# Performance work log

Measured on AMD Instinct MI355X. Metric: run time of the kernel, lower is better.

The kernel has to match this reference:

```python
import jax, jax.numpy as jnp
import numpy as np

B, S, D, H = 2, 2048, 1024, 16
HD = D // H  # head_dim = 64
SCALE = HD ** -0.5


def setup_inputs() -> dict:
    key = jax.random.key(0)
    ks = jax.random.split(key, 10)
    std = D ** -0.5
    return {
        "x": jax.random.normal(ks[0], (B, S, D), jnp.float32),
        "y": jax.random.normal(ks[1], (B, S, D), jnp.float32),
        "Wq": jax.random.normal(ks[2], (D, D), jnp.float32) * std,
        "bq": jnp.zeros((D,), jnp.float32),
        "Wk": jax.random.normal(ks[3], (D, D), jnp.float32) * std,
        "bk": jnp.zeros((D,), jnp.float32),
        "Wv": jax.random.normal(ks[4], (D, D), jnp.float32) * std,
        "bv": jnp.zeros((D,), jnp.float32),
        "Wo": jax.random.normal(ks[5], (D, D), jnp.float32) * std,
        "bo": jnp.zeros((D,), jnp.float32),
    }


def reference(x, y, Wq, bq, Wk, bk, Wv, bv, Wo, bo):
    # Linear projections (torch Linear: x @ W.T + b; here W stored as [in,out])
    q = x @ Wq + bq  # [B,S,D]
    k = y @ Wk + bk
    v = y @ Wv + bv
    # split heads -> [B,H,S,hd]
    q = q.reshape(B, S, H, HD).transpose(0, 2, 1, 3)
    k = k.reshape(B, S, H, HD).transpose(0, 2, 1, 3)
    v = v.reshape(B, S, H, HD).transpose(0, 2, 1, 3)
    scores = jnp.einsum("bhqd,bhkd->bhqk", q, k) * SCALE  # [B,H,S,S]
    causal = jnp.tril(jnp.ones((S, S), dtype=bool))  # keep lower triangle
    scores = jnp.where(causal[None, None], scores, -jnp.inf)
    attn = jax.nn.softmax(scores, axis=-1)
    out = jnp.einsum("bhqk,bhkd->bhqd", attn, v)  # [B,H,S,hd]
    out = out.transpose(0, 2, 1, 3).reshape(B, S, D)
    return out @ Wo + bo
```

## Files before the change

kernel.cpp:

```cpp
#include <hip/hip_runtime.h>
#include <hip/hip_bf16.h>


#define BDIM 2
#define SDIM 2048
#define DDIM 1024
#define HDIM 16
#define HD   64
#define MDIM (BDIM*SDIM)
#define C2 0.18033688011112042f

using short8  = __attribute__((ext_vector_type(8))) short;
using floatx4 = __attribute__((ext_vector_type(4))) float;

static __device__ __forceinline__ unsigned short f2bf(float x) {
    union { float f; unsigned int u; } c; c.f = x;
    unsigned int r = (c.u + 0x7fffu + ((c.u >> 16) & 1u)) >> 16;
    return (unsigned short)r;
}

static __device__ __forceinline__ unsigned int pack2bf(float a, float b) {
    union { float f; unsigned int u; } ua, ub;
    ua.f = a; ub.f = b;
    return __builtin_amdgcn_perm(ub.u + 0x8000u, ua.u + 0x8000u, 0x07060302u);
}

#define GLD16(g, l) __builtin_amdgcn_global_load_lds(                        \
    (const __attribute__((address_space(1))) void*)(g),                      \
    (__attribute__((address_space(3))) void*)(l), 16, 0, 0)

__global__ __launch_bounds__(256) void prep_kernel(
    const float* __restrict__ X, const float* __restrict__ Y,
    const float* __restrict__ W0, const float* __restrict__ W1,
    const float* __restrict__ W2, const float* __restrict__ W3,
    unsigned short* __restrict__ Xo, unsigned short* __restrict__ Yo,
    unsigned short* __restrict__ T0, unsigned short* __restrict__ T1,
    unsigned short* __restrict__ T2, unsigned short* __restrict__ T3)
{
    __shared__ float tile[64][68];
    const int z = blockIdx.z;
    const int t = threadIdx.x;
    if (z < 2) {
        const float* A    = z ? Y : X;
        unsigned short* O = z ? Yo : Xo;
        const int idx = blockIdx.x * 256 + t;
        const float4 a = ((const float4*)A)[idx*2];
        const float4 b = ((const float4*)A)[idx*2 + 1];
        ushort4 lo, hi;
        lo.x = f2bf(a.x); lo.y = f2bf(a.y); lo.z = f2bf(a.z); lo.w = f2bf(a.w);
        hi.x = f2bf(b.x); hi.y = f2bf(b.y); hi.z = f2bf(b.z); hi.w = f2bf(b.w);
        ((ushort4*)O)[idx*2]     = lo;
        ((ushort4*)O)[idx*2 + 1] = hi;
        return;
    }
    if (blockIdx.x >= 256) return;
    const int zz = z - 2;
    const float* W    = (zz == 0) ? W0 : (zz == 1) ? W1 : (zz == 2) ? W2 : W3;
    unsigned short* T = (zz == 0) ? T0 : (zz == 1) ? T1 : (zz == 2) ? T2 : T3;
    const int k0 = (blockIdx.x & 15) * 64, n0 = (blockIdx.x >> 4) * 64;
    #pragma unroll
    for (int i = 0; i < 4; ++i) {
        const int idx = t + i*256;
        const int kr = idx >> 4, c4 = idx & 15;
        float4 v = *(const float4*)&W[(size_t)(k0 + kr) * DDIM + n0 + c4*4];
        tile[kr][c4*4+0] = v.x; tile[kr][c4*4+1] = v.y;
        tile[kr][c4*4+2] = v.z; tile[kr][c4*4+3] = v.w;
    }
    __syncthreads();
    #pragma unroll
    for (int i = 0; i < 4; ++i) {
        const int idx = t + i*256;
        const int nr = idx >> 4, kc = idx & 15;
        ushort4 o;
        o.x = f2bf(tile[kc*4+0][nr]); o.y = f2bf(tile[kc*4+1][nr]);
        o.z = f2bf(tile[kc*4+2][nr]); o.w = f2bf(tile[kc*4+3][nr]);
        *(ushort4*)&T[(size_t)(n0 + nr) * DDIM + k0 + kc*4] = o;
    }
}

template <bool SWAP>
__device__ __forceinline__ void gemm128_core(
    const unsigned short* __restrict__ A, const unsigned short* __restrict__ Bt,
    int bm, int bn, unsigned short* As, unsigned short* Bs, floatx4 acc[4][4])
{
    const int t = threadIdx.x;
    const int w = t >> 6, l = t & 63;
    const int quad = l >> 4, col = l & 15;
    const int wr = (w >> 1) * 64, wc = (w & 1) * 64;

    const int c1 = t + 256;
    const int r0 = t >> 2,  o0 = (t & 3) * 8;
    const int r1 = c1 >> 2, o1 = (c1 & 3) * 8;

    const unsigned short* Ar0 = A  + (size_t)(bm + r0) * DDIM + o0;
    const unsigned short* Ar1 = A  + (size_t)(bm + r1) * DDIM + o1;
    const unsigned short* Br0 = Bt + (size_t)(bn + r0) * DDIM + o0;
    const unsigned short* Br1 = Bt + (size_t)(bn + r1) * DDIM + o1;

    GLD16(Ar0, As + t*8);
    GLD16(Ar1, As + c1*8);
    GLD16(Br0, Bs + t*8);
    GLD16(Br1, Bs + c1*8);

    for (int kt = 0; kt < DDIM; kt += 32) {
        const int cur = (kt >> 5) & 1;
        unsigned short* Asn = As + (cur ^ 1) * 4096;
        unsigned short* Bsn = Bs + (cur ^ 1) * 4096;
        __syncthreads();
        if (kt + 32 < DDIM) {
            GLD16(Ar0 + kt + 32, Asn + t*8);
            GLD16(Ar1 + kt + 32, Asn + c1*8);
            GLD16(Br0 + kt + 32, Bsn + t*8);
            GLD16(Br1 + kt + 32, Bsn + c1*8);
        }
        const unsigned short* Asc = As + cur*4096;
        const unsigned short* Bsc = Bs + cur*4096;
        short8 af[4], bfr[4];
        #pragma unroll
        for (int i = 0; i < 4; ++i)
            af[i] = *(const short8*)&Asc[(wr + i*16 + col)*32 + quad*8];
        #pragma unroll
        for (int j = 0; j < 4; ++j)
            bfr[j] = *(const short8*)&Bsc[(wc + j*16 + col)*32 + quad*8];
        #pragma unroll
        for (int i = 0; i < 4; ++i)
            #pragma unroll
            for (int j = 0; j < 4; ++j)
                acc[i][j] = SWAP
                    ? __builtin_amdgcn_mfma_f32_16x16x32_bf16(bfr[j], af[i], acc[i][j], 0, 0, 0)
                    : __builtin_amdgcn_mfma_f32_16x16x32_bf16(af[i], bfr[j], acc[i][j], 0, 0, 0);
    }
}

__global__ __launch_bounds__(256) void qkv_gemm_kernel(
    const unsigned short* __restrict__ xbf, const unsigned short* __restrict__ ybf,
    const unsigned short* __restrict__ Wqt, const unsigned short* __restrict__ Wkt,
    const unsigned short* __restrict__ Wvt,
    const float* __restrict__ bq, const float* __restrict__ bk,
    const float* __restrict__ bv,
    unsigned short* __restrict__ Qbf, unsigned short* __restrict__ Kbf,
    unsigned short* __restrict__ vT)
{
    __shared__ __align__(16) unsigned short As[2*4096];
    __shared__ __align__(16) unsigned short Bs[2*4096];

    const int z = blockIdx.z;
    const unsigned short* A  = (z == 0) ? xbf : ybf;
    const unsigned short* Wt = (z == 0) ? Wqt : (z == 1) ? Wkt : Wvt;
    const float* bp          = (z == 0) ? bq  : (z == 1) ? bk  : bv;

    const int bm = (blockIdx.x * 4 + (blockIdx.y & 3)) * 128;
    const int bn = (blockIdx.y >> 2) * 128;

    const int t = threadIdx.x;
    const int w = t >> 6, l = t & 63;
    const int quad = l >> 4, col = l & 15;
    const int wr = (w >> 1) * 64, wc = (w & 1) * 64;

    floatx4 acc[4][4] = {};

    if (z < 2) {
        gemm128_core<true>(A, Wt, bm, bn, As, Bs, acc);
        unsigned short* O = (z == 0) ? Qbf : Kbf;
        const float sc = (z == 0) ? C2 : 1.0f;
        float4 bias4[4];
        #pragma unroll
        for (int j = 0; j < 4; ++j)
            bias4[j] = *(const float4*)&bp[bn + wc + j*16 + quad*4];
        #pragma unroll
        for (int i = 0; i < 4; ++i) {
            const int m = bm + wr + i*16 + col;
            unsigned short* rowp = O + (size_t)m * DDIM;
            #pragma unroll
            for (int j = 0; j < 4; ++j) {
                const float v0 = (acc[i][j][0] + bias4[j].x) * sc;
                const float v1 = (acc[i][j][1] + bias4[j].y) * sc;
                const float v2 = (acc[i][j][2] + bias4[j].z) * sc;
                const float v3 = (acc[i][j][3] + bias4[j].w) * sc;
                uint2 pk;
                pk.x = pack2bf(v0, v1);
                pk.y = pack2bf(v2, v3);
                *(uint2*)&rowp[bn + wc + j*16 + quad*4] = pk;
            }
        }
    } else {
        gemm128_core<false>(A, Wt, bm, bn, As, Bs, acc);
        #pragma unroll
        for (int j = 0; j < 4; ++j) {
            const int gn = bn + wc + j*16 + col;
            const float bias = bp[gn];
            #pragma unroll
            for (int i = 0; i < 4; ++i) {
                const int gm0 = bm + wr + i*16 + quad*4;
                uint2 pk;
                pk.x = pack2bf(acc[i][j][0] + bias, acc[i][j][1] + bias);
                pk.y = pack2bf(acc[i][j][2] + bias, acc[i][j][3] + bias);
                *(uint2*)&vT[((size_t)((gm0 >> 11) * DDIM + gn)) * SDIM + (gm0 & 2047)] = pk;
            }
        }
    }
}

__global__ __launch_bounds__(256) void out_gemm_kernel(
    const unsigned short* __restrict__ Obf, const unsigned short* __restrict__ Wot,
    const float* __restrict__ bo, float* __restrict__ out)
{
    __shared__ __align__(16) unsigned short As[2*4096];
    __shared__ __align__(16) unsigned short Bs[2*2048];

    const int t = threadIdx.x;
    const int w = t >> 6, l = t & 63;
    const int quad = l >> 4, col = l & 15;

    const int j  = (blockIdx.x >> 3) + 2 * blockIdx.y;
    const int bm = ((blockIdx.x & 7) * 4 + (j & 3)) * 128;
    const int bn = (j >> 2) * 64;

    const int wr = (w >> 1) * 64, wc = (w & 1) * 32;

    const int r0 = t >> 2, o0 = (t & 3) * 8;
    const unsigned short* Ar0 = Obf + (size_t)(bm + r0) * DDIM + o0;
    const unsigned short* Ar1 = Obf + (size_t)(bm + 64 + r0) * DDIM + o0;
    const unsigned short* Br  = Wot + (size_t)(bn + r0) * DDIM + o0;

    floatx4 acc[4][2] = {};

    GLD16(Ar0, As + t*8);
    GLD16(Ar1, As + (t + 256)*8);
    GLD16(Br,  Bs + t*8);

    for (int kt = 0; kt < DDIM; kt += 32) {
        const int cur = (kt >> 5) & 1;
        unsigned short* Asn = As + (cur ^ 1) * 4096;
        unsigned short* Bsn = Bs + (cur ^ 1) * 2048;
        __syncthreads();
        if (kt + 32 < DDIM) {
            GLD16(Ar0 + kt + 32, Asn + t*8);
            GLD16(Ar1 + kt + 32, Asn + (t + 256)*8);
            GLD16(Br  + kt + 32, Bsn + t*8);
        }
        const unsigned short* Asc = As + cur*4096;
        const unsigned short* Bsc = Bs + cur*2048;
        short8 af[4], bfr[2];
        #pragma unroll
        for (int i = 0; i < 4; ++i)
            af[i] = *(const short8*)&Asc[(wr + i*16 + col)*32 + quad*8];
        #pragma unroll
        for (int j2 = 0; j2 < 2; ++j2)
            bfr[j2] = *(const short8*)&Bsc[(wc + j2*16 + col)*32 + quad*8];
        #pragma unroll
        for (int i = 0; i < 4; ++i)
            #pragma unroll
            for (int j2 = 0; j2 < 2; ++j2)
                acc[i][j2] = __builtin_amdgcn_mfma_f32_16x16x32_bf16(
                    bfr[j2], af[i], acc[i][j2], 0, 0, 0);
    }

    float4 bias4[2];
    #pragma unroll
    for (int j2 = 0; j2 < 2; ++j2)
        bias4[j2] = *(const float4*)&bo[bn + wc + j2*16 + quad*4];
    #pragma unroll
    for (int i = 0; i < 4; ++i) {
        const int m = bm + wr + i*16 + col;
        float* rowp = out + (size_t)m * DDIM;
        #pragma unroll
        for (int j2 = 0; j2 < 2; ++j2) {
            float4 o;
            o.x = acc[i][j2][0] + bias4[j2].x;
            o.y = acc[i][j2][1] + bias4[j2].y;
            o.z = acc[i][j2][2] + bias4[j2].z;
            o.w = acc[i][j2][3] + bias4[j2].w;
            *(float4*)&rowp[bn + wc + j2*16 + quad*4] = o;
        }
    }
}

__global__ __launch_bounds__(256, 2) void attn_mfma_kernel(
    const unsigned short* __restrict__ Qbf, const unsigned short* __restrict__ Kbf,
    const unsigned short* __restrict__ vT, unsigned short* __restrict__ Obf)
{
    __shared__ float ls[2][4*64];
    __shared__ __align__(16) floatx4 os[2][1024];

    const int t = threadIdx.x;
    const int w = t >> 6, l = t & 63;
    const int quad = l >> 4, col = l & 15;

    const int lin = blockIdx.x;
    const int j   = lin >> 3, rem = j & 3;
    const int qt  = 31 - (j >> 2);
    const int b   = rem & 1;
    const int h   = (lin & 7) + 8 * (rem >> 1);

    const size_t hoff = (size_t)h * HD;
    const size_t bS   = (size_t)b * SDIM;
    const size_t bD   = (size_t)b * DDIM;
    const int qb = qt * 64;

    short8 qf[4][2];
    #pragma unroll
    for (int m = 0; m < 4; ++m)
        #pragma unroll
        for (int hf = 0; hf < 2; ++hf)
            qf[m][hf] = *(const short8*)
                &Qbf[(bS + qb + m*16 + col) * DDIM + hoff + hf*32 + quad*8];

    floatx4 o[4][4] = {};
    float lrun[4] = {0.f, 0.f, 0.f, 0.f};

    const int rowp = ((col >> 2) << 3) | (col & 3);
    const unsigned short* kb0 = Kbf + bS * DDIM + hoff + quad*8;
    const unsigned short* vb0 = vT + (bD + hoff + col) * SDIM + quad*8;

    #pragma unroll 1
    for (int it = w; it <= qt; it += 4) {
        const int ktb = it * 64;
        const bool diag = (it == qt);

        short8 kf[2][2][2];
        #pragma unroll
        for (int c = 0; c < 2; ++c)
            #pragma unroll
            for (int tt = 0; tt < 2; ++tt) {
                const size_t row = (size_t)(ktb + c*32 + tt*4 + rowp);
                kf[c][tt][0] = *(const short8*)&kb0[row * DDIM];
                kf[c][tt][1] = *(const short8*)&kb0[row * DDIM + 32];
            }
        short8 vf[4][2];
        #pragma unroll
        for (int n = 0; n < 4; ++n)
            #pragma unroll
            for (int c = 0; c < 2; ++c)
                vf[n][c] = *(const short8*)
                    &vb0[(size_t)(n*16) * SDIM + ktb + c*32];

        #pragma unroll
        for (int m = 0; m < 4; ++m) {
            #pragma unroll
            for (int c = 0; c < 2; ++c) {
                if (diag && (c*32 > m*16 + 15)) continue;
                const bool needm = diag && (c*32 + 31 > m*16);

                floatx4 s0 = {}, s1 = {};
                __builtin_amdgcn_s_setprio(1);
                s0 = __builtin_amdgcn_mfma_f32_16x16x32_bf16(kf[c][0][0], qf[m][0], s0, 0, 0, 0);
                s0 = __builtin_amdgcn_mfma_f32_16x16x32_bf16(kf[c][0][1], qf[m][1], s0, 0, 0, 0);
                s1 = __builtin_amdgcn_mfma_f32_16x16x32_bf16(kf[c][1][0], qf[m][0], s1, 0, 0, 0);
                s1 = __builtin_amdgcn_mfma_f32_16x16x32_bf16(kf[c][1][1], qf[m][1], s1, 0, 0, 0);
                __builtin_amdgcn_s_setprio(0);

                float p0[4], p1[4];
                const int qrow = m*16 + col;
                const int kls  = c*32 + quad*8;
                #pragma unroll
                for (int r = 0; r < 4; ++r) {
                    p0[r] = (needm && (kls + r     > qrow)) ? 0.0f : exp2f(s0[r]);
                    p1[r] = (needm && (kls + 4 + r > qrow)) ? 0.0f : exp2f(s1[r]);
                }
                lrun[m] += ((p0[0]+p0[1]) + (p0[2]+p0[3]))
                         + ((p1[0]+p1[1]) + (p1[2]+p1[3]));

                union { short8 v; unsigned int u[4]; } pf;
                pf.u[0] = pack2bf(p0[0], p0[1]);
                pf.u[1] = pack2bf(p0[2], p0[3]);
                pf.u[2] = pack2bf(p1[0], p1[1]);
                pf.u[3] = pack2bf(p1[2], p1[3]);

                __builtin_amdgcn_s_setprio(1);
                #pragma unroll
                for (int n = 0; n < 4; ++n)
                    o[n][m] = __builtin_amdgcn_mfma_f32_16x16x32_bf16(
                        vf[n][c], pf.v, o[n][m], 0, 0, 0);
                __builtin_amdgcn_s_setprio(0);
            }
        }
    }

    if (w >= 2) {
        const int s = w - 2;
        #pragma unroll
        for (int n = 0; n < 4; ++n)
            #pragma unroll
            for (int m = 0; m < 4; ++m)
                os[s][(n*4 + m)*64 + l] = o[n][m];
        #pragma unroll
        for (int m = 0; m < 4; ++m)
            ls[s][m*64 + l] = lrun[m];
    }
    __syncthreads();
    if (w < 2) {
        #pragma unroll
        for (int n = 0; n < 4; ++n)
            #pragma unroll
            for (int m = 0; m < 4; ++m)
                o[n][m] += os[w][(n*4 + m)*64 + l];
        #pragma unroll
        for (int m = 0; m < 4; ++m)
            lrun[m] += ls[w][m*64 + l];
    }
    __syncthreads();
    if (w == 1) {
        #pragma unroll
        for (int n = 0; n < 4; ++n)
            #pragma unroll
            for (int m = 0; m < 4; ++m)
                os[0][(n*4 + m)*64 + l] = o[n][m];
        #pragma unroll
        for (int m = 0; m < 4; ++m)
            ls[0][m*64 + l] = lrun[m];
    }
    __syncthreads();
    if (w == 0) {
        #pragma unroll
        for (int m = 0; m < 4; ++m) {
            float lt = lrun[m] + ls[0][m*64 + l];
            lt += __shfl_xor(lt, 16);
            lt += __shfl_xor(lt, 32);
            const float inv = 1.0f / lt;
            #pragma unroll
            for (int n = 0; n < 4; ++n) {
                const floatx4 ov = o[n][m] + os[0][(n*4 + m)*64 + l];
                uint2 pk;
                pk.x = pack2bf(ov[0] * inv, ov[1] * inv);
                pk.y = pack2bf(ov[2] * inv, ov[3] * inv);
                *(uint2*)&Obf[(bS + qb + m*16 + col) * DDIM
                              + hoff + n*16 + quad*4] = pk;
            }
        }
    }
}

extern "C" void kernel_launch(void* const* d_in, const int* in_sizes, int n_in,
                              void* d_out, int out_size, void* d_ws, size_t ws_size,
                              hipStream_t stream) {
    const float* x  = (const float*)d_in[0];
    const float* y  = (const float*)d_in[1];
    const float* Wq = (const float*)d_in[2];
    const float* bq = (const float*)d_in[3];
    const float* Wk = (const float*)d_in[4];
    const float* bk = (const float*)d_in[5];
    const float* Wv = (const float*)d_in[6];
    const float* bv = (const float*)d_in[7];
    const float* Wo = (const float*)d_in[8];
    const float* bo = (const float*)d_in[9];
    float* out = (float*)d_out;

    const size_t mat  = (size_t)MDIM * DDIM;
    const size_t wmat = (size_t)DDIM * DDIM;
    unsigned short* p = (unsigned short*)d_ws;
    unsigned short* xbf = p;            p += mat;
    unsigned short* ybf = p;            p += mat;
    unsigned short* Wqt = p;            p += wmat;
    unsigned short* Wkt = p;            p += wmat;
    unsigned short* Wvt = p;            p += wmat;
    unsigned short* Wot = p;            p += wmat;
    unsigned short* Qbf = p;            p += mat;
    unsigned short* Kbf = p;            p += mat;
    unsigned short* vT  = p;            p += mat;
    unsigned short* Obf = p;            p += mat;

    hipLaunchKernelGGL(prep_kernel, dim3(MDIM*DDIM/8/256, 1, 6), dim3(256),
                       0, stream, x, y, Wq, Wk, Wv, Wo,
                       xbf, ybf, Wqt, Wkt, Wvt, Wot);

    hipLaunchKernelGGL(qkv_gemm_kernel, dim3(DDIM/128, MDIM/128, 3), dim3(256),
                       0, stream, xbf, ybf, Wqt, Wkt, Wvt, bq, bk, bv,
                       Qbf, Kbf, vT);

    hipLaunchKernelGGL(attn_mfma_kernel, dim3(1024), dim3(256),
                       0, stream, Qbf, Kbf, vT, Obf);

    hipLaunchKernelGGL(out_gemm_kernel, dim3(DDIM/64, MDIM/128), dim3(256),
                       0, stream, Obf, Wot, bo, out);
}
```

Before: 208.5 us.

## Pair causal query tiles per block and double-buffer K fragment loads

Each attention block now handles two query tiles, one long (31-p) and one short (p), so every block does roughly equal causal work and the grid halves from 1024 to 512 blocks. The inner key loop also prefetches the next iteration's K fragments into a second register buffer while computing the current one. The aim is to remove the tail imbalance of the causal triangle and to hide global-load latency. The cost is higher register pressure from the double buffer, an extra block-wide sync per phase, and fewer blocks for the scheduler to balance.

```diff
diff --git a/kernel.cpp b/kernel.cpp
--- a/kernel.cpp
+++ b/kernel.cpp
@@ -288,146 +288,168 @@
     const int quad = l >> 4, col = l & 15;
 
     const int lin = blockIdx.x;
-    const int j   = lin >> 3, rem = j & 3;
-    const int qt  = 31 - (j >> 2);
+    const int r   = lin >> 3, rem = r & 3;
+    const int p   = r >> 2;
     const int b   = rem & 1;
     const int h   = (lin & 7) + 8 * (rem >> 1);
 
     const size_t hoff = (size_t)h * HD;
     const size_t bS   = (size_t)b * SDIM;
     const size_t bD   = (size_t)b * DDIM;
-    const int qb = qt * 64;
-
-    short8 qf[4][2];
-    #pragma unroll
-    for (int m = 0; m < 4; ++m)
-        #pragma unroll
-        for (int hf = 0; hf < 2; ++hf)
-            qf[m][hf] = *(const short8*)
-                &Qbf[(bS + qb + m*16 + col) * DDIM + hoff + hf*32 + quad*8];
-
-    floatx4 o[4][4] = {};
-    float lrun[4] = {0.f, 0.f, 0.f, 0.f};
 
     const int rowp = ((col >> 2) << 3) | (col & 3);
     const unsigned short* kb0 = Kbf + bS * DDIM + hoff + quad*8;
     const unsigned short* vb0 = vT + (bD + hoff + col) * SDIM + quad*8;
 
     #pragma unroll 1
-    for (int it = w; it <= qt; it += 4) {
-        const int ktb = it * 64;
-        const bool diag = (it == qt);
-
-        short8 kf[2][2][2];
-        #pragma unroll
-        for (int c = 0; c < 2; ++c)
-            #pragma unroll
-            for (int tt = 0; tt < 2; ++tt) {
-                const size_t row = (size_t)(ktb + c*32 + tt*4 + rowp);
-                kf[c][tt][0] = *(const short8*)&kb0[row * DDIM];
-                kf[c][tt][1] = *(const short8*)&kb0[row * DDIM + 32];
+    for (int ph = 0; ph < 2; ++ph) {
+        const int qT = ph ? p : (31 - p);
+        const int qb = qT * 64;
+
+        short8 qf[4][2];
+        #pragma unroll
+        for (int m = 0; m < 4; ++m)
+            #pragma unroll
+            for (int hf = 0; hf < 2; ++hf)
+                qf[m][hf] = *(const short8*)
+                    &Qbf[(bS + qb + m*16 + col) * DDIM + hoff + hf*32 + quad*8];
+
+        floatx4 o[4][4] = {};
+        float lrun[4] = {0.f, 0.f, 0.f, 0.f};
+
+        auto loadK = [&](short8 kf[2][2][2], int it) {
+            const int ktb = it * 64;
+            #pragma unroll
+            for (int c = 0; c < 2; ++c)
+                #pragma unroll
+                for (int tt = 0; tt < 2; ++tt) {
+                    const size_t row = (size_t)(ktb + c*32 + tt*4 + rowp);
+                    kf[c][tt][0] = *(const short8*)&kb0[row * DDIM];
+                    kf[c][tt][1] = *(const short8*)&kb0[row * DDIM + 32];
+                }
+        };
+
+        auto compute = [&](short8 kf[2][2][2], int it) {
+            const int ktb = it * 64;
+            const bool diag = (it == qT);
+            short8 vf[4][2];
+            #pragma unroll
+            for (int n = 0; n < 4; ++n)
+                #pragma unroll
+                for (int c = 0; c < 2; ++c)
+                    vf[n][c] = *(const short8*)
+                        &vb0[(size_t)(n*16) * SDIM + ktb + c*32];
+
+            #pragma unroll
+            for (int m = 0; m < 4; ++m) {
+                #pragma unroll
+                for (int c = 0; c < 2; ++c) {
+                    if (diag && (c*32 > m*16 + 15)) continue;
+                    const bool needm = diag && (c*32 + 31 > m*16);
+
+                    floatx4 s0 = {}, s1 = {};
+                    __builtin_amdgcn_s_setprio(1);
+                    s0 = __builtin_amdgcn_mfma_f32_16x16x32_bf16(kf[c][0][0], qf[m][0], s0, 0, 0, 0);
+                    s0 = __builtin_amdgcn_mfma_f32_16x16x32_bf16(kf[c][0][1], qf[m][1], s0, 0, 0, 0);
+                    s1 = __builtin_amdgcn_mfma_f32_16x16x32_bf16(kf[c][1][0], qf[m][0], s1, 0, 0, 0);
+                    s1 = __builtin_amdgcn_mfma_f32_16x16x32_bf16(kf[c][1][1], qf[m][1], s1, 0, 0, 0);
+                    __builtin_amdgcn_s_setprio(0);
+
+                    float p0[4], p1[4];
+                    const int qrow = m*16 + col;
+                    const int kls  = c*32 + quad*8;
+                    #pragma unroll
+                    for (int rr = 0; rr < 4; ++rr) {
+                        p0[rr] = (needm && (kls + rr     > qrow)) ? 0.0f : exp2f(s0[rr]);
+                        p1[rr] = (needm && (kls + 4 + rr > qrow)) ? 0.0f : exp2f(s1[rr]);
+                    }
+                    lrun[m] += ((p0[0]+p0[1]) + (p0[2]+p0[3]))
+                             + ((p1[0]+p1[1]) + (p1[2]+p1[3]));
+
+                    union { short8 v; unsigned int u[4]; } pf;
+                    pf.u[0] = pack2bf(p0[0], p0[1]);
+                    pf.u[1] = pack2bf(p0[2], p0[3]);
+                    pf.u[2] = pack2bf(p1[0], p1[1]);
+                    pf.u[3] = pack2bf(p1[2], p1[3]);
+
+                    __builtin_amdgcn_s_setprio(1);
+                    #pragma unroll
+                    for (int n = 0; n < 4; ++n)
+                        o[n][m] = __builtin_amdgcn_mfma_f32_16x16x32_bf16(
+                            vf[n][c], pf.v, o[n][m], 0, 0, 0);
+                    __builtin_amdgcn_s_setprio(0);
+                }
             }
-        short8 vf[4][2];
-        #pragma unroll
-        for (int n = 0; n < 4; ++n)
-            #pragma unroll
-            for (int c = 0; c < 2; ++c)
-                vf[n][c] = *(const short8*)
-                    &vb0[(size_t)(n*16) * SDIM + ktb + c*32];
-
-        #pragma unroll
-        for (int m = 0; m < 4; ++m) {
-            #pragma unroll
-            for (int c = 0; c < 2; ++c) {
-                if (diag && (c*32 > m*16 + 15)) continue;
-                const bool needm = diag && (c*32 + 31 > m*16);
-
-                floatx4 s0 = {}, s1 = {};
-                __builtin_amdgcn_s_setprio(1);
-                s0 = __builtin_amdgcn_mfma_f32_16x16x32_bf16(kf[c][0][0], qf[m][0], s0, 0, 0, 0);
-                s0 = __builtin_amdgcn_mfma_f32_16x16x32_bf16(kf[c][0][1], qf[m][1], s0, 0, 0, 0);
-                s1 = __builtin_amdgcn_mfma_f32_16x16x32_bf16(kf[c][1][0], qf[m][0], s1, 0, 0, 0);
-                s1 = __builtin_amdgcn_mfma_f32_16x16x32_bf16(kf[c][1][1], qf[m][1], s1, 0, 0, 0);
-                __builtin_amdgcn_s_setprio(0);
-
-                float p0[4], p1[4];
-                const int qrow = m*16 + col;
-                const int kls  = c*32 + quad*8;
-                #pragma unroll
-                for (int r = 0; r < 4; ++r) {
-                    p0[r] = (needm && (kls + r     > qrow)) ? 0.0f : exp2f(s0[r]);
-                    p1[r] = (needm && (kls + 4 + r > qrow)) ? 0.0f : exp2f(s1[r]);
+        };
+
+        {
+            short8 kfA[2][2][2], kfB[2][2][2];
+            int it = w;
+            if (it <= qT) loadK(kfA, it);
+            while (it <= qT) {
+                if (it + 4 <= qT) loadK(kfB, it + 4);
+                compute(kfA, it);
+                it += 4;
+                if (it > qT) break;
+                if (it + 4 <= qT) loadK(kfA, it + 4);
+                compute(kfB, it);
+                it += 4;
+            }
+        }
+
+        if (w >= 2) {
+            const int s = w - 2;
+            #pragma unroll
+            for (int n = 0; n < 4; ++n)
+                #pragma unroll
+                for (int m = 0; m < 4; ++m)
+                    os[s][(n*4 + m)*64 + l] = o[n][m];
+            #pragma unroll
+            for (int m = 0; m < 4; ++m)
+                ls[s][m*64 + l] = lrun[m];
+        }
+        __syncthreads();
+        if (w < 2) {
+            #pragma unroll
+            for (int n = 0; n < 4; ++n)
+                #pragma unroll
+                for (int m = 0; m < 4; ++m)
+                    o[n][m] += os[w][(n*4 + m)*64 + l];
+            #pragma unroll
+            for (int m = 0; m < 4; ++m)
+                lrun[m] += ls[w][m*64 + l];
+        }
+        __syncthreads();
+        if (w == 1) {
+            #pragma unroll
+            for (int n = 0; n < 4; ++n)
+                #pragma unroll
+                for (int m = 0; m < 4; ++m)
+                    os[0][(n*4 + m)*64 + l] = o[n][m];
+            #pragma unroll
+            for (int m = 0; m < 4; ++m)
+                ls[0][m*64 + l] = lrun[m];
+        }
+        __syncthreads();
+        if (w == 0) {
+            #pragma unroll
+            for (int m = 0; m < 4; ++m) {
+                float lt = lrun[m] + ls[0][m*64 + l];
+                lt += __shfl_xor(lt, 16);
+                lt += __shfl_xor(lt, 32);
+                const float inv = 1.0f / lt;
+                #pragma unroll
+                for (int n = 0; n < 4; ++n) {
+                    const floatx4 ov = o[n][m] + os[0][(n*4 + m)*64 + l];
+                    uint2 pk;
+                    pk.x = pack2bf(ov[0] * inv, ov[1] * inv);
+                    pk.y = pack2bf(ov[2] * inv, ov[3] * inv);
+                    *(uint2*)&Obf[(bS + qb + m*16 + col) * DDIM
+                                  + hoff + n*16 + quad*4] = pk;
                 }
-                lrun[m] += ((p0[0]+p0[1]) + (p0[2]+p0[3]))
-                         + ((p1[0]+p1[1]) + (p1[2]+p1[3]));
-
-                union { short8 v; unsigned int u[4]; } pf;
-                pf.u[0] = pack2bf(p0[0], p0[1]);
-                pf.u[1] = pack2bf(p0[2], p0[3]);
-                pf.u[2] = pack2bf(p1[0], p1[1]);
-                pf.u[3] = pack2bf(p1[2], p1[3]);
-
-                __builtin_amdgcn_s_setprio(1);
-                #pragma unroll
-                for (int n = 0; n < 4; ++n)
-                    o[n][m] = __builtin_amdgcn_mfma_f32_16x16x32_bf16(
-                        vf[n][c], pf.v, o[n][m], 0, 0, 0);
-                __builtin_amdgcn_s_setprio(0);
             }
         }
-    }
-
-    if (w >= 2) {
-        const int s = w - 2;
-        #pragma unroll
-        for (int n = 0; n < 4; ++n)
-            #pragma unroll
-            for (int m = 0; m < 4; ++m)
-                os[s][(n*4 + m)*64 + l] = o[n][m];
-        #pragma unroll
-        for (int m = 0; m < 4; ++m)
-            ls[s][m*64 + l] = lrun[m];
-    }
-    __syncthreads();
-    if (w < 2) {
-        #pragma unroll
-        for (int n = 0; n < 4; ++n)
-            #pragma unroll
-            for (int m = 0; m < 4; ++m)
-                o[n][m] += os[w][(n*4 + m)*64 + l];
-        #pragma unroll
-        for (int m = 0; m < 4; ++m)
-            lrun[m] += ls[w][m*64 + l];
-    }
-    __syncthreads();
-    if (w == 1) {
-        #pragma unroll
-        for (int n = 0; n < 4; ++n)
-            #pragma unroll
-            for (int m = 0; m < 4; ++m)
-                os[0][(n*4 + m)*64 + l] = o[n][m];
-        #pragma unroll
-        for (int m = 0; m < 4; ++m)
-            ls[0][m*64 + l] = lrun[m];
-    }
-    __syncthreads();
-    if (w == 0) {
-        #pragma unroll
-        for (int m = 0; m < 4; ++m) {
-            float lt = lrun[m] + ls[0][m*64 + l];
-            lt += __shfl_xor(lt, 16);
-            lt += __shfl_xor(lt, 32);
-            const float inv = 1.0f / lt;
-            #pragma unroll
-            for (int n = 0; n < 4; ++n) {
-                const floatx4 ov = o[n][m] + os[0][(n*4 + m)*64 + l];
-                uint2 pk;
-                pk.x = pack2bf(ov[0] * inv, ov[1] * inv);
-                pk.y = pack2bf(ov[2] * inv, ov[3] * inv);
-                *(uint2*)&Obf[(bS + qb + m*16 + col) * DDIM
-                              + hoff + n*16 + quad*4] = pk;
-            }
-        }
+        __syncthreads();
     }
 }
 
@@ -468,7 +490,7 @@
                        0, stream, xbf, ybf, Wqt, Wkt, Wvt, bq, bk, bv,
                        Qbf, Kbf, vT);
 
-    hipLaunchKernelGGL(attn_mfma_kernel, dim3(1024), dim3(256),
+    hipLaunchKernelGGL(attn_mfma_kernel, dim3(512), dim3(256),
                        0, stream, Qbf, Kbf, vT, Obf);
 
     hipLaunchKernelGGL(out_gemm_kernel, dim3(DDIM/64, MDIM/128), dim3(256),
```

New measurement: 294.4 us. +41.2%, slower.
